# Kernel optimization log

Hardware: AMD Instinct MI355X
Metric: run time of the kernel (lower is better)

Reference implementation:

```python
import jax, jax.numpy as jnp
import numpy as np
from jax import lax

_SIGMAS = [0.5, 1.0, 2.0, 4.0, 8.0]
_FS = int(4 * _SIGMAS[-1] + 1)   # 33
_PAD = int(2 * _SIGMAS[-1])      # 16
_C1 = (0.01 * 1.0) ** 2
_C2 = (0.03 * 1.0) ** 2
_ALPHA = 0.025
_COMP = 200.0
_DR = 1.0


def _gauss2d(size, sigma):
    coords = np.arange(size, dtype=np.float32) - size // 2
    g = np.exp(-coords ** 2 / (2.0 * sigma ** 2))
    g /= g.sum()
    return np.outer(g, g).astype(np.float32)


def _build_g_masks():
    g = np.zeros((3 * len(_SIGMAS), 1, _FS, _FS), dtype=np.float32)
    for i, s in enumerate(_SIGMAS):
        k = _gauss2d(_FS, s)
        for j in range(3):
            g[3 * i + j, 0] = k
    return jnp.asarray(g)


def setup_inputs() -> dict:
    key = jax.random.key(0)
    kx, ky = jax.random.split(key)
    B, C, H, W = 8, 3, 512, 512
    x = jax.random.uniform(kx, (B, C, H, W), dtype=jnp.float32)
    y = jax.random.uniform(ky, (B, C, H, W), dtype=jnp.float32)
    return {"x": x, "y": y, "g_masks": _build_g_masks()}


def _gconv(img, w):
    # grouped conv, 3 groups (one per RGB channel), 'same' padding of 16
    return lax.conv_general_dilated(
        img, w, window_strides=(1, 1), padding=[(_PAD, _PAD), (_PAD, _PAD)],
        dimension_numbers=("NCHW", "OIHW", "NCHW"), feature_group_count=3)


def reference(x, y, g_masks):
    mux = _gconv(x, g_masks)            # [B,15,H,W]
    muy = _gconv(y, g_masks)
    mux2 = mux * mux
    muy2 = muy * muy
    muxy = mux * muy
    sigmax2 = _gconv(x * x, g_masks) - mux2
    sigmay2 = _gconv(y * y, g_masks) - muy2
    sigmaxy = _gconv(x * y, g_masks) - muxy

    l = (2.0 * muxy + _C1) / (mux2 + muy2 + _C1)
    cs = (2.0 * sigmaxy + _C2) / (sigmax2 + sigmay2 + _C2)

    lM = l[:, -1] * l[:, -2] * l[:, -3]   # largest-sigma luminance terms
    PIcs = jnp.prod(cs, axis=1)
    loss_ms_ssim = 1.0 - lM * PIcs        # [B,H,W]

    loss_l1 = jnp.abs(x - y)              # [B,3,H,W]
    gaussian_l1 = _gconv(loss_l1, g_masks[-3:]).mean(axis=1)  # [B,H,W]

    loss_mix = _ALPHA * loss_ms_ssim + (1.0 - _ALPHA) * gaussian_l1 / _DR
    return (_COMP * loss_mix).mean()
```

## Files before the change

kernel.cpp:

```cpp
#include <hip/hip_runtime.h>

typedef _Float16 h2_t __attribute__((ext_vector_type(2)));
typedef _Float16 f16x8 __attribute__((ext_vector_type(8)));
typedef float f32x4 __attribute__((ext_vector_type(4)));
typedef unsigned u32x4 __attribute__((ext_vector_type(4)));

#define DI __device__ __forceinline__

#if __has_builtin(__builtin_amdgcn_sched_barrier)
#define SCHED_FENCE() __builtin_amdgcn_sched_barrier(0)
#else
#define SCHED_FENCE()
#endif

constexpr int PAW = 96;
constexpr int PBV = 72;
constexpr int TILE = 64 * PAW;
constexpr int PLANE = 64 * PBV;
constexpr float kC1 = 1.0e-4f;
constexpr float kC2 = 9.0e-4f;
constexpr float kALPHA = 0.025f;

DI float rcp_fast(float v) { return __builtin_amdgcn_rcpf(v); }

DI float fdot2f(h2_t a, h2_t b, float c) {
#if __has_builtin(__builtin_amdgcn_fdot2)
  return __builtin_amdgcn_fdot2(a, b, c, false);
#else
  return c + (float)(a.x) * (float)(b.x) + (float)(a.y) * (float)(b.y);
#endif
}

DI h2_t w2h(unsigned u) { return __builtin_bit_cast(h2_t, u); }

DI f16x8 ldfrag(const _Float16* __restrict__ p) {
  return *reinterpret_cast<const f16x8*>(p);
}

DI f32x4 mfma16(f16x8 a, f16x8 b, f32x4 c) {
  return __builtin_amdgcn_mfma_f32_16x16x32_f16(a, b, c, 0, 0, 0);
}

DI f16x8 pkabs8(f16x8 v) {
  u32x4 u = __builtin_bit_cast(u32x4, v);
  u32x4 msk = {0x7FFF7FFFu, 0x7FFF7FFFu, 0x7FFF7FFFu, 0x7FFF7FFFu};
  u &= msk;
  return __builtin_bit_cast(f16x8, u);
}

template<int PASS>
DI void hconv_m(const _Float16* __restrict__ xt, _Float16* __restrict__ hb,
                f16x8 wA0, f16x8 wA1, int w, int lane) {
  const int q = lane >> 4, m = lane & 15;
  const int K0b = (w < 2) ? 0 : 32;
  const int cb = w * 16 + q * 4;
  f32x4 zero4 = {0.f, 0.f, 0.f, 0.f};
#pragma unroll
  for (int nt = 0; nt < 4; ++nt) {
    const int row = nt * 16 + m;
    const int base = row * PAW + K0b + q * 8;
    f32x4 a0 = zero4, a1 = zero4;
#pragma unroll
    for (int ks = 0; ks < 2; ++ks) {
      const f16x8 A = ks ? wA1 : wA0;
      const int idx = (base + ks * 32) ^ ((row & 7) << 3);
      f16x8 xv = ldfrag(xt + idx);
      f16x8 yv = ldfrag(xt + TILE + idx);
      if (PASS == 0) {
        a0 = mfma16(A, xv, a0);
        a1 = mfma16(A, yv, a1);
      } else if (PASS == 1) {
        f16x8 sq = xv * xv + yv * yv;
        f16x8 xy = xv * yv;
        a0 = mfma16(A, sq, a0);
        a1 = mfma16(A, xy, a1);
      } else {
        a0 = mfma16(A, pkabs8(xv - yv), a0);
      }
    }
    _Float16* wp = hb + cb * PBV + nt * 16 + m;
#pragma unroll
    for (int j = 0; j < 4; ++j) {
      wp[j * PBV] = (_Float16)a0[j];
      if (PASS < 2) wp[PLANE + j * PBV] = (_Float16)a1[j];
    }
    SCHED_FENCE();
  }
}

DI void vconv_m(const _Float16* __restrict__ hb,
                f16x8 w00, f16x8 w01, f16x8 w10, f16x8 w11,
                int w, int lane, float* __restrict__ o0, float* __restrict__ o1) {
  const int q = lane >> 4, m = lane & 15;
  const int base = (w * 16 + m) * PBV + q * 8;
  f32x4 zero4 = {0.f, 0.f, 0.f, 0.f};
  f32x4 a00 = zero4, a01 = zero4, a10 = zero4, a11 = zero4;
#pragma unroll
  for (int ks = 0; ks < 2; ++ks) {
    f16x8 A0 = ldfrag(hb + base + ks * 32);
    f16x8 A1 = ldfrag(hb + PLANE + base + ks * 32);
    f16x8 B0 = ks ? w01 : w00;
    f16x8 B1 = ks ? w11 : w10;
    a00 = mfma16(A0, B0, a00);
    a01 = mfma16(A0, B1, a01);
    a10 = mfma16(A1, B0, a10);
    a11 = mfma16(A1, B1, a11);
    SCHED_FENCE();
  }
#pragma unroll
  for (int j = 0; j < 4; ++j) {
    o0[j] = a00[j]; o0[4 + j] = a01[j];
    o1[j] = a10[j]; o1[4 + j] = a11[j];
  }
}

DI float vl1(const _Float16* __restrict__ hb, const unsigned* __restrict__ U,
             int col, int r0) {
  const _Float16* p0 = hb + col * PBV + r0;
  float s = 0.f;
#pragma unroll
  for (int p = 0; p < 20; ++p)
    s = fdot2f(w2h(U[p]), *reinterpret_cast<const h2_t*>(p0 + 2 * p), s);
  return s;
}

template<bool LAST>
DI void do_sigma_m(int s, const _Float16* __restrict__ frh,
                   const unsigned* __restrict__ U,
                   const _Float16* __restrict__ xt, _Float16* __restrict__ hb,
                   float* __restrict__ PIcs, float& gl1s, int tid) {
  const int lane = tid & 63, w = tid >> 6;
  const f16x8* fr = reinterpret_cast<const f16x8*>(frh) + s * 256 + lane;
  f16x8 w00 = fr[0], w01 = fr[64], w10 = fr[128], w11 = fr[192];
  const bool odd = (w & 1);
  f16x8 wA0 = odd ? w10 : w00;
  f16x8 wA1 = odd ? w11 : w01;

  hconv_m<0>(xt, hb, wA0, wA1, w, lane);
  __syncthreads();
  float mux[8], muy[8];
  vconv_m(hb, w00, w01, w10, w11, w, lane, mux, muy);
  __syncthreads();
  hconv_m<1>(xt, hb, wA0, wA1, w, lane);
  __syncthreads();
  float s2[8], exy[8];
  vconv_m(hb, w00, w01, w10, w11, w, lane, s2, exy);
  __syncthreads();
#pragma unroll
  for (int i = 0; i < 8; ++i) {
    float a = mux[i], b = muy[i];
    float m2 = a * a + b * b, mxy = a * b;
    PIcs[i] *= fmaf(2.f, exy[i] - mxy, kC2) * rcp_fast(s2[i] - m2 + kC2);
    if (LAST)
      PIcs[i] *= fmaf(2.f, mxy, kC1) * rcp_fast(m2 + kC1);
  }
  if (LAST) {
    hconv_m<2>(xt, hb, wA0, wA1, w, lane);
    __syncthreads();
    gl1s += vl1(hb, U, tid & 63, (tid >> 6) * 8);
    __syncthreads();
  }
}

DI unsigned packh(float a, float b) {
  h2_t v; v.x = (_Float16)a; v.y = (_Float16)b;
  return __builtin_bit_cast(unsigned, v);
}

__global__ void prep_k(const float* __restrict__ gm, float* __restrict__ ws) {
  int t = threadIdx.x;
  if (t < 165) {
    int s = t / 33, j = t % 33;
    const float* mk = gm + (3 * s) * (33 * 33);
    ws[t] = mk[16 * 33 + j] / sqrtf(mk[16 * 33 + 16]);
  }
  __syncthreads();
  if (t == 0) {
    const float* w = ws + 4 * 33;
    unsigned* U = (unsigned*)(ws + 168);
    for (int p = 0; p < 20; ++p) {
      float ux = 0.f, uy = 0.f;
      for (int i = 0; i < 4; ++i) {
        int j = p - i;
        if (j < 0 || j > 16) continue;
        ux += w[2 * j];
        if (2 * j + 1 <= 32) uy += w[2 * j + 1];
        if (j > 0) ux += w[2 * j - 1];
        uy += w[2 * j];
      }
      U[p] = packh(ux, uy);
    }
  }
  _Float16* fr = (_Float16*)(ws + 208);
  const int Rs[5] = {4, 6, 12, 16, 16};
  for (int e = t; e < 10240; e += 256) {
    int s = e >> 11, r = e & 2047;
    int cls = (r >> 10) & 1, ks = (r >> 9) & 1, lane = (r >> 3) & 63, i = r & 7;
    int tp = 32 * ks - 16 * cls + 8 * (lane >> 4) + i - (lane & 15);
    int R = Rs[s], j = tp - 16 + R;
    float v = (j >= 0 && j <= 2 * R) ? ws[s * 33 + j] : 0.f;
    fr[e] = (_Float16)v;
  }
}

__global__ __launch_bounds__(256, 2)
void msloss_k(const float* __restrict__ x, const float* __restrict__ y,
              const float* __restrict__ ws, float* __restrict__ out) {
  __shared__ __align__(16) _Float16 smem[2 * TILE + 2 * PLANE];
  __shared__ float red[4];
  _Float16* xt = smem;
  _Float16* hb = smem + 2 * TILE;
  const _Float16* frh = (const _Float16*)(ws + 208);
  const unsigned* U = (const unsigned*)(ws + 168);
  const int tid = threadIdx.x;
  const int ox = blockIdx.x * 64, oy = blockIdx.y * 32;
  const int b = blockIdx.z;

  float PIcs[8];
  float gl1s = 0.f;
#pragma unroll
  for (int i = 0; i < 8; ++i) PIcs[i] = 1.f;

  for (int c = 0; c < 3; ++c) {
    const float* xp = x + (size_t)(b * 3 + c) * (512 * 512);
    const float* yp = y + (size_t)(b * 3 + c) * (512 * 512);
#pragma unroll
    for (int it = 0; it < 12; ++it) {
      int idx = it * 256 + tid;
      int row = idx / 48, cp = idx % 48;
      int gy = oy + row - 16, gx = ox + cp * 2 - 16;
      bool ok = ((unsigned)gy < 512u) && ((unsigned)gx < 512u);
      float2 xv = make_float2(0.f, 0.f), yv = make_float2(0.f, 0.f);
      if (ok) {
        xv = *reinterpret_cast<const float2*>(xp + gy * 512 + gx);
        yv = *reinterpret_cast<const float2*>(yp + gy * 512 + gx);
      }
      h2_t hx; hx.x = (_Float16)xv.x; hx.y = (_Float16)xv.y;
      h2_t hy; hy.x = (_Float16)yv.x; hy.y = (_Float16)yv.y;
      int si = (row * PAW + cp * 2) ^ ((row & 7) << 3);
      *reinterpret_cast<h2_t*>(xt + si) = hx;
      *reinterpret_cast<h2_t*>(xt + TILE + si) = hy;
    }
    __syncthreads();
    do_sigma_m<false>(0, frh, U, xt, hb, PIcs, gl1s, tid);
    do_sigma_m<false>(1, frh, U, xt, hb, PIcs, gl1s, tid);
    do_sigma_m<false>(2, frh, U, xt, hb, PIcs, gl1s, tid);
    do_sigma_m<false>(3, frh, U, xt, hb, PIcs, gl1s, tid);
    do_sigma_m<true >(4, frh, U, xt, hb, PIcs, gl1s, tid);
  }

  float s = ((1.f - kALPHA) / 3.f) * gl1s;
#pragma unroll
  for (int i = 0; i < 8; ++i) s += kALPHA * (1.f - PIcs[i]);
#pragma unroll
  for (int off = 32; off > 0; off >>= 1) s += __shfl_down(s, off);
  if ((tid & 63) == 0) red[tid >> 6] = s;
  __syncthreads();
  if (tid == 0)
    atomicAdd(out, (red[0] + red[1] + red[2] + red[3]) *
                       (200.0f / (8.0f * 512.0f * 512.0f)));
}

extern "C" void kernel_launch(void* const* d_in, const int* in_sizes, int n_in,
                              void* d_out, int out_size, void* d_ws, size_t ws_size,
                              hipStream_t stream) {
  const float* x = (const float*)d_in[0];
  const float* y = (const float*)d_in[1];
  const float* gm = (const float*)d_in[2];
  float* out = (float*)d_out;
  float* ws = (float*)d_ws;

  hipMemsetAsync(d_out, 0, out_size * sizeof(float), stream);
  prep_k<<<1, 256, 0, stream>>>(gm, ws);
  msloss_k<<<dim3(8, 16, 8), 256, 0, stream>>>(x, y, ws, out);
}
```

Measured before the change: 289.8 us.

## Fuse all horizontal/vertical conv passes per sigma into one with five planes

Merges the separate horizontal and vertical MFMA convolution passes (means, second moments, L1) into a single horizontal pass that writes up to five intermediate planes, followed by one vertical pass. This cuts the barrier count per sigma from four to six down to two, and the input tile is loaded from LDS once instead of two or three times. In exchange LDS use grows from 2 to 5 intermediate planes (about 66 KB per block). More accumulators are live at once, which raises register pressure and may reduce occupancy below the 2 blocks per CU that launch_bounds requests.

```diff
diff --git a/kernel.cpp b/kernel.cpp
--- a/kernel.cpp
+++ b/kernel.cpp
@@ -48,9 +48,9 @@
   return __builtin_bit_cast(f16x8, u);
 }
 
-template<int PASS>
-DI void hconv_m(const _Float16* __restrict__ xt, _Float16* __restrict__ hb,
-                f16x8 wA0, f16x8 wA1, int w, int lane) {
+template<bool L1P>
+DI void hconv_all(const _Float16* __restrict__ xt, _Float16* __restrict__ hb,
+                  f16x8 wA0, f16x8 wA1, int w, int lane) {
   const int q = lane >> 4, m = lane & 15;
   const int K0b = (w < 2) ? 0 : 32;
   const int cb = w * 16 + q * 4;
@@ -59,64 +59,54 @@
   for (int nt = 0; nt < 4; ++nt) {
     const int row = nt * 16 + m;
     const int base = row * PAW + K0b + q * 8;
-    f32x4 a0 = zero4, a1 = zero4;
+    f32x4 ax = zero4, ay = zero4, asq = zero4, axy = zero4, al1 = zero4;
 #pragma unroll
     for (int ks = 0; ks < 2; ++ks) {
       const f16x8 A = ks ? wA1 : wA0;
       const int idx = (base + ks * 32) ^ ((row & 7) << 3);
       f16x8 xv = ldfrag(xt + idx);
       f16x8 yv = ldfrag(xt + TILE + idx);
-      if (PASS == 0) {
-        a0 = mfma16(A, xv, a0);
-        a1 = mfma16(A, yv, a1);
-      } else if (PASS == 1) {
-        f16x8 sq = xv * xv + yv * yv;
-        f16x8 xy = xv * yv;
-        a0 = mfma16(A, sq, a0);
-        a1 = mfma16(A, xy, a1);
-      } else {
-        a0 = mfma16(A, pkabs8(xv - yv), a0);
-      }
+      ax = mfma16(A, xv, ax);
+      ay = mfma16(A, yv, ay);
+      asq = mfma16(A, xv * xv + yv * yv, asq);
+      axy = mfma16(A, xv * yv, axy);
+      if (L1P) al1 = mfma16(A, pkabs8(xv - yv), al1);
     }
     _Float16* wp = hb + cb * PBV + nt * 16 + m;
 #pragma unroll
     for (int j = 0; j < 4; ++j) {
-      wp[j * PBV] = (_Float16)a0[j];
-      if (PASS < 2) wp[PLANE + j * PBV] = (_Float16)a1[j];
+      wp[j * PBV] = (_Float16)ax[j];
+      wp[PLANE + j * PBV] = (_Float16)ay[j];
+      wp[2 * PLANE + j * PBV] = (_Float16)asq[j];
+      wp[3 * PLANE + j * PBV] = (_Float16)axy[j];
+      if (L1P) wp[4 * PLANE + j * PBV] = (_Float16)al1[j];
     }
     SCHED_FENCE();
   }
 }
 
-DI void vconv_m(const _Float16* __restrict__ hb,
-                f16x8 w00, f16x8 w01, f16x8 w10, f16x8 w11,
-                int w, int lane, float* __restrict__ o0, float* __restrict__ o1) {
+DI void vconv_all(const _Float16* __restrict__ hb,
+                  f16x8 w00, f16x8 w01, f16x8 w10, f16x8 w11,
+                  int w, int lane, f32x4* __restrict__ acc) {
   const int q = lane >> 4, m = lane & 15;
   const int base = (w * 16 + m) * PBV + q * 8;
-  f32x4 zero4 = {0.f, 0.f, 0.f, 0.f};
-  f32x4 a00 = zero4, a01 = zero4, a10 = zero4, a11 = zero4;
 #pragma unroll
   for (int ks = 0; ks < 2; ++ks) {
-    f16x8 A0 = ldfrag(hb + base + ks * 32);
-    f16x8 A1 = ldfrag(hb + PLANE + base + ks * 32);
     f16x8 B0 = ks ? w01 : w00;
     f16x8 B1 = ks ? w11 : w10;
-    a00 = mfma16(A0, B0, a00);
-    a01 = mfma16(A0, B1, a01);
-    a10 = mfma16(A1, B0, a10);
-    a11 = mfma16(A1, B1, a11);
+#pragma unroll
+    for (int pl = 0; pl < 4; ++pl) {
+      f16x8 A = ldfrag(hb + pl * PLANE + base + ks * 32);
+      acc[2 * pl]     = mfma16(A, B0, acc[2 * pl]);
+      acc[2 * pl + 1] = mfma16(A, B1, acc[2 * pl + 1]);
+    }
     SCHED_FENCE();
-  }
-#pragma unroll
-  for (int j = 0; j < 4; ++j) {
-    o0[j] = a00[j]; o0[4 + j] = a01[j];
-    o1[j] = a10[j]; o1[4 + j] = a11[j];
   }
 }
 
 DI float vl1(const _Float16* __restrict__ hb, const unsigned* __restrict__ U,
              int col, int r0) {
-  const _Float16* p0 = hb + col * PBV + r0;
+  const _Float16* p0 = hb + 4 * PLANE + col * PBV + r0;
   float s = 0.f;
 #pragma unroll
   for (int p = 0; p < 20; ++p)
@@ -136,30 +126,27 @@
   f16x8 wA0 = odd ? w10 : w00;
   f16x8 wA1 = odd ? w11 : w01;
 
-  hconv_m<0>(xt, hb, wA0, wA1, w, lane);
-  __syncthreads();
-  float mux[8], muy[8];
-  vconv_m(hb, w00, w01, w10, w11, w, lane, mux, muy);
-  __syncthreads();
-  hconv_m<1>(xt, hb, wA0, wA1, w, lane);
-  __syncthreads();
-  float s2[8], exy[8];
-  vconv_m(hb, w00, w01, w10, w11, w, lane, s2, exy);
-  __syncthreads();
-#pragma unroll
-  for (int i = 0; i < 8; ++i) {
-    float a = mux[i], b = muy[i];
-    float m2 = a * a + b * b, mxy = a * b;
-    PIcs[i] *= fmaf(2.f, exy[i] - mxy, kC2) * rcp_fast(s2[i] - m2 + kC2);
-    if (LAST)
-      PIcs[i] *= fmaf(2.f, mxy, kC1) * rcp_fast(m2 + kC1);
-  }
-  if (LAST) {
-    hconv_m<2>(xt, hb, wA0, wA1, w, lane);
-    __syncthreads();
-    gl1s += vl1(hb, U, tid & 63, (tid >> 6) * 8);
-    __syncthreads();
-  }
+  hconv_all<LAST>(xt, hb, wA0, wA1, w, lane);
+  __syncthreads();
+  f32x4 zero4 = {0.f, 0.f, 0.f, 0.f};
+  f32x4 acc[8];
+#pragma unroll
+  for (int i = 0; i < 8; ++i) acc[i] = zero4;
+  vconv_all(hb, w00, w01, w10, w11, w, lane, acc);
+  if (LAST) gl1s += vl1(hb, U, tid & 63, (tid >> 6) * 8);
+#pragma unroll
+  for (int h = 0; h < 2; ++h)
+#pragma unroll
+    for (int j = 0; j < 4; ++j) {
+      const int i = h * 4 + j;
+      float a = acc[h][j], b = acc[2 + h][j];
+      float m2 = a * a + b * b, mxy = a * b;
+      PIcs[i] *= fmaf(2.f, acc[6 + h][j] - mxy, kC2) *
+                 rcp_fast(acc[4 + h][j] - m2 + kC2);
+      if (LAST)
+        PIcs[i] *= fmaf(2.f, mxy, kC1) * rcp_fast(m2 + kC1);
+    }
+  __syncthreads();
 }
 
 DI unsigned packh(float a, float b) {
@@ -206,7 +193,7 @@
 __global__ __launch_bounds__(256, 2)
 void msloss_k(const float* __restrict__ x, const float* __restrict__ y,
               const float* __restrict__ ws, float* __restrict__ out) {
-  __shared__ __align__(16) _Float16 smem[2 * TILE + 2 * PLANE];
+  __shared__ __align__(16) _Float16 smem[2 * TILE + 5 * PLANE];
   __shared__ float red[4];
   _Float16* xt = smem;
   _Float16* hb = smem + 2 * TILE;
```

Result: faster. 275.8 us (-4.9%).
